# Kernel optimization log

Hardware: AMD Instinct MI355X
Metric: run time of the kernel (lower is better)

Reference implementation:

```python
import jax, jax.numpy as jnp
import numpy as np

DIM = 768
NUM_HEADS = 12
HEAD_DIM = DIM // NUM_HEADS
SCALE = HEAD_DIM ** -0.5


def setup_inputs() -> dict:
    key = jax.random.key(0)
    ks = jax.random.split(key, 9)
    B, N = 2, 4096
    s = DIM ** -0.5
    return {
        "query": jax.random.normal(ks[0], (B, N, DIM), jnp.float32),
        "key": jax.random.normal(ks[1], (B, N, DIM), jnp.float32),
        "value": jax.random.normal(ks[2], (B, N, DIM), jnp.float32),
        "Wq": jax.random.normal(ks[3], (DIM, DIM), jnp.float32) * s,
        "Wk": jax.random.normal(ks[4], (DIM, DIM), jnp.float32) * s,
        "bk": jax.random.normal(ks[5], (DIM,), jnp.float32) * 0.02,
        "Wv": jax.random.normal(ks[6], (DIM, DIM), jnp.float32) * s,
        "Wp": jax.random.normal(ks[7], (DIM, DIM), jnp.float32) * s,
        "bp": jax.random.normal(ks[8], (DIM,), jnp.float32) * 0.02,
    }


def reference(query, key, value, Wq, Wk, bk, Wv, Wp, bp):
    B, Nq, C = query.shape
    Nk = key.shape[1]
    H, D = NUM_HEADS, HEAD_DIM
    # QKV projections (qv_bias=False -> no bias on q, v; k has bias)
    q = (query @ Wq.T).reshape(B, Nq, H, D).transpose(0, 2, 1, 3)  # [B,H,Nq,D]
    k = (key @ Wk.T + bk).reshape(B, Nk, H, D).transpose(0, 2, 1, 3)
    v = (value @ Wv.T).reshape(B, Nk, H, D).transpose(0, 2, 1, 3)
    # non-standard: exact GELU applied to K before QK^T
    k = jax.nn.gelu(k, approximate=False)
    attn = jnp.einsum("bhqd,bhkd->bhqk", q, k) * SCALE
    attn = jax.nn.softmax(attn, axis=-1)
    x = jnp.einsum("bhqk,bhkd->bhqd", attn, v)
    x = x.transpose(0, 2, 1, 3).reshape(B, Nq, C)
    return x @ Wp.T + bp
```

## Files before the change

kernel.cpp:

```cpp
#include <hip/hip_runtime.h>
#include <hip/hip_bf16.h>


#define DIM 768
#define NH 12
#define HD 64
#define NTOK 4096
#define WELEM 589824u
#define TELEM 6291456u

typedef short bf16x8 __attribute__((ext_vector_type(8)));
typedef float floatx4 __attribute__((ext_vector_type(4)));
typedef unsigned short us4 __attribute__((ext_vector_type(4)));

__device__ __forceinline__ float bf2f(unsigned short u) {
    union { unsigned int i; float f; } v; v.i = ((unsigned int)u) << 16; return v.f;
}
__device__ __forceinline__ unsigned short f2bf(float f) {
    union { float f; unsigned int i; } v; v.f = f;
    unsigned int r = v.i + 0x7fffu + ((v.i >> 16) & 1u);
    return (unsigned short)(r >> 16);
}
__device__ __forceinline__ unsigned int packbf(float a, float b) {
    __hip_bfloat162 h = __float22bfloat162_rn(make_float2(a, b));
    union { __hip_bfloat162 h; unsigned int u; } cv; cv.h = h; return cv.u;
}
__device__ __forceinline__ void gl2lds16(const unsigned short* g, unsigned short* l) {
    __builtin_amdgcn_global_load_lds(
        (const __attribute__((address_space(1))) unsigned int*)g,
        (__attribute__((address_space(3))) unsigned int*)l, 16, 0, 0);
}
__device__ __forceinline__ bf16x8 ld8_f32_to_bf16(const float* p) {
    floatx4 f0 = *(const floatx4*)p;
    floatx4 f1 = *(const floatx4*)(p + 4);
    union { unsigned int u[4]; bf16x8 v; } o;
    o.u[0] = packbf(f0[0], f0[1]);
    o.u[1] = packbf(f0[2], f0[3]);
    o.u[2] = packbf(f1[0], f1[1]);
    o.u[3] = packbf(f1[2], f1[3]);
    return o.v;
}

#if __has_builtin(__builtin_amdgcn_exp2f)
#define EXPFN(x) __builtin_amdgcn_exp2f(x)
#define QSCALE 0.18033688011f
#else
#define EXPFN(x) __expf(x)
#define QSCALE 0.125f
#endif

__global__ __launch_bounds__(256) void cvt_w(
    const float* __restrict__ a, const float* __restrict__ b,
    const float* __restrict__ c, const float* __restrict__ d,
    unsigned short* __restrict__ dst)
{
    size_t i = ((size_t)blockIdx.x * 256 + threadIdx.x) * 8;
    const float* s; size_t off;
    if (i < WELEM)            { s = a; off = i; }
    else if (i < 2u * WELEM)  { s = b; off = i - WELEM; }
    else if (i < 3u * WELEM)  { s = c; off = i - 2u * WELEM; }
    else                      { s = d; off = i - 3u * WELEM; }
    *(bf16x8*)(dst + i) = ld8_f32_to_bf16(s + off);
}

__global__ __launch_bounds__(256) void cvt_in(
    const float* __restrict__ a, const float* __restrict__ b,
    const float* __restrict__ c, unsigned short* __restrict__ dst)
{
    size_t i = ((size_t)blockIdx.x * 256 + threadIdx.x) * 8;
    const float* s; size_t off;
    if (i < TELEM)            { s = a; off = i; }
    else if (i < 2u * TELEM)  { s = b; off = i - TELEM; }
    else                      { s = c; off = i - 2u * TELEM; }
    *(bf16x8*)(dst + i) = ld8_f32_to_bf16(s + off);
}

template <int A_IS_BF16>
__device__ __forceinline__ void gemm128(
    const void* __restrict__ Av, const unsigned short* __restrict__ W,
    const float* __restrict__ bias, void* __restrict__ Cv,
    int has_bias, int do_gelu, int trans, int out_f32)
{
    __shared__ unsigned short As[128 * 64];
    __shared__ unsigned short Bs[128 * 64];
    const int m0 = blockIdx.x * 128, n0 = blockIdx.y * 128;
    const int tid = threadIdx.x;
    const int w = tid >> 6, l = tid & 63;
    const int g = l >> 4, r16 = l & 15;
    const int wm = w >> 1, wn = w & 1;
    const int ro = l >> 3, c = l & 7;
    const int cswz = ((c ^ ro) & 7) * 8;

    floatx4 acc[4][4];
#pragma unroll
    for (int i = 0; i < 4; i++)
#pragma unroll
        for (int j = 0; j < 4; j++) acc[i][j] = (floatx4){0.f, 0.f, 0.f, 0.f};

    for (int k0 = 0; k0 < DIM; k0 += 64) {
#pragma unroll
        for (int q = 0; q < 4; q++) {
            int rbase = w * 32 + q * 8;
            if (A_IS_BF16) {
                gl2lds16((const unsigned short*)Av + (size_t)(m0 + rbase + ro) * DIM + k0 + cswz,
                         As + rbase * 64);
            } else {
                bf16x8 a = ld8_f32_to_bf16((const float*)Av + (size_t)(m0 + rbase + ro) * DIM + k0 + c * 8);
                *(bf16x8*)(As + (rbase + ro) * 64 + cswz) = a;
            }
            gl2lds16(W + (size_t)(n0 + rbase + ro) * DIM + k0 + cswz, Bs + rbase * 64);
        }
        __syncthreads();

#pragma unroll
        for (int kk = 0; kk < 2; kk++) {
            bf16x8 af[4], bfr[4];
            int x = r16 & 7;
#pragma unroll
            for (int i = 0; i < 4; i++)
                af[i] = *(const bf16x8*)(As + (wm * 64 + i * 16 + r16) * 64 + (((kk * 4 + g) ^ x) * 8));
#pragma unroll
            for (int j = 0; j < 4; j++)
                bfr[j] = *(const bf16x8*)(Bs + (wn * 64 + j * 16 + r16) * 64 + (((kk * 4 + g) ^ x) * 8));
#pragma unroll
            for (int i = 0; i < 4; i++)
#pragma unroll
                for (int j = 0; j < 4; j++)
                    acc[i][j] = __builtin_amdgcn_mfma_f32_16x16x32_bf16(af[i], bfr[j], acc[i][j], 0, 0, 0);
        }
        __syncthreads();
    }

    if (trans) {
        unsigned short* C = (unsigned short*)Cv;
#pragma unroll
        for (int i = 0; i < 4; i++) {
            int m = m0 + wm * 64 + i * 16 + g * 4;
            int b = m >> 12, tloc = m & 4095;
#pragma unroll
            for (int j = 0; j < 4; j++) {
                int n = n0 + wn * 64 + j * 16 + r16;
                int h = n >> 6, d = n & 63;
                union { unsigned int u[2]; us4 v; } pk;
                pk.u[0] = packbf(acc[i][j][0], acc[i][j][1]);
                pk.u[1] = packbf(acc[i][j][2], acc[i][j][3]);
                *(us4*)(C + ((size_t)(b * NH + h) * 64 + d) * NTOK + tloc) = pk.v;
            }
        }
    } else {
#pragma unroll
        for (int i = 0; i < 4; i++)
#pragma unroll
            for (int j = 0; j < 4; j++) {
                int n = n0 + wn * 64 + j * 16 + r16;
                float bv = has_bias ? bias[n] : 0.f;
#pragma unroll
                for (int r = 0; r < 4; r++) {
                    int m = m0 + wm * 64 + i * 16 + g * 4 + r;
                    float v = acc[i][j][r] + bv;
                    if (do_gelu) v = 0.5f * v * (1.f + erff(v * 0.70710678118f));
                    if (out_f32) ((float*)Cv)[(size_t)m * DIM + n] = v;
                    else ((unsigned short*)Cv)[(size_t)m * DIM + n] = f2bf(v);
                }
            }
    }
}

template <int A_IS_BF16>
__global__ __launch_bounds__(256) void qkv_gemm(
    const void* __restrict__ q_in, const void* __restrict__ k_in,
    const void* __restrict__ v_in,
    const unsigned short* __restrict__ Wq, const unsigned short* __restrict__ Wk,
    const unsigned short* __restrict__ Wv, const float* __restrict__ bk,
    unsigned short* __restrict__ Qo, unsigned short* __restrict__ Ko,
    unsigned short* __restrict__ Vto)
{
    int z = blockIdx.z;
    const void* A = (z == 0) ? q_in : (z == 1) ? k_in : v_in;
    const unsigned short* W = (z == 0) ? Wq : (z == 1) ? Wk : Wv;
    unsigned short* C = (z == 0) ? Qo : (z == 1) ? Ko : Vto;
    gemm128<A_IS_BF16>(A, W, bk, C, z == 1, z == 1, z == 2, 0);
}

__global__ __launch_bounds__(256) void out_gemm(
    const unsigned short* __restrict__ X, const unsigned short* __restrict__ Wp,
    const float* __restrict__ bp, float* __restrict__ out)
{
    gemm128<1>(X, Wp, bp, out, 1, 0, 0, 1);
}

__device__ __forceinline__ int swzf(int R) { return (R & 7) ^ ((R >> 2) & 6); }

__global__ __launch_bounds__(128, 2) void attn_kernel(
    const unsigned short* __restrict__ Q, const unsigned short* __restrict__ K,
    const unsigned short* __restrict__ Vt, unsigned short* __restrict__ X)
{
    __shared__ unsigned short Ks[2][64 * 64];
    __shared__ unsigned short Vs[2][64 * 64];
    const int qt = blockIdx.x, bh = blockIdx.y;
    const int b = bh / NH, h = bh % NH;
    const int tid = threadIdx.x;
    const int w = tid >> 6, l = tid & 63;
    const int g = l >> 4, r16 = l & 15;
    const int tokbase = b * NTOK;

    bf16x8 qfr[4][2];
#pragma unroll
    for (int qfi = 0; qfi < 4; qfi++) {
        int qrow = tokbase + qt * 128 + w * 64 + qfi * 16 + r16;
#pragma unroll
        for (int kk = 0; kk < 2; kk++) {
            bf16x8 t = *(const bf16x8*)(Q + (size_t)qrow * DIM + h * HD + kk * 32 + g * 8);
#pragma unroll
            for (int j = 0; j < 8; j++)
                t[j] = (short)f2bf(bf2f((unsigned short)t[j]) * QSCALE);
            qfr[qfi][kk] = t;
        }
    }

    int koff[4][2], voff[4][2];
#pragma unroll
    for (int ct = 0; ct < 4; ct++) {
        int krow = (ct >> 1) * 32 + (r16 >> 2) * 8 + (ct & 1) * 4 + (r16 & 3);
#pragma unroll
        for (int kk = 0; kk < 2; kk++)
            koff[ct][kk] = krow * 64 + (((kk * 4 + g) ^ swzf(krow)) * 8);
    }
#pragma unroll
    for (int dt = 0; dt < 4; dt++) {
        int vrow = dt * 16 + r16;
#pragma unroll
        for (int c = 0; c < 2; c++)
            voff[dt][c] = vrow * 64 + (((c * 4 + g) ^ swzf(vrow)) * 8);
    }

    int soff[8];
    const int srl = l >> 3, scc = l & 7;
    const int sstride = (w == 0) ? DIM : NTOK;
#pragma unroll
    for (int i = 0; i < 8; i++) {
        int row = i * 8 + srl;
        soff[i] = row * sstride + ((scc ^ swzf(row)) * 8);
    }
    const unsigned short* Kbase = K + (size_t)tokbase * DIM + h * HD;
    const unsigned short* Vbase = Vt + (size_t)bh * 64 * NTOK;

    floatx4 o[4][4];
#pragma unroll
    for (int qfi = 0; qfi < 4; qfi++)
#pragma unroll
        for (int dt = 0; dt < 4; dt++) o[qfi][dt] = (floatx4){0.f, 0.f, 0.f, 0.f};
    float lsum[4] = {0.f, 0.f, 0.f, 0.f};

    {
        const unsigned short* p = (w == 0) ? Kbase : Vbase;
        unsigned short* dst = (w == 0) ? Ks[0] : Vs[0];
#pragma unroll
        for (int i = 0; i < 8; i++) gl2lds16(p + soff[i], dst + i * 512);
    }

    for (int kt = 0; kt < NTOK / 64; kt++) {
        const int cur = kt & 1;
        __syncthreads();

        bf16x8 kr[4][2], vr[4][2];
#pragma unroll
        for (int ct = 0; ct < 4; ct++)
#pragma unroll
            for (int kk = 0; kk < 2; kk++)
                kr[ct][kk] = *(const bf16x8*)(Ks[cur] + koff[ct][kk]);
#pragma unroll
        for (int dt = 0; dt < 4; dt++)
#pragma unroll
            for (int c = 0; c < 2; c++)
                vr[dt][c] = *(const bf16x8*)(Vs[cur] + voff[dt][c]);

        if (kt + 1 < NTOK / 64) {
            int keyg = (kt + 1) * 64;
            const unsigned short* p = (w == 0) ? (Kbase + (size_t)keyg * DIM)
                                               : (Vbase + keyg);
            unsigned short* dst = (w == 0) ? Ks[cur ^ 1] : Vs[cur ^ 1];
#pragma unroll
            for (int i = 0; i < 8; i++) gl2lds16(p + soff[i], dst + i * 512);
        }

#pragma unroll
        for (int qfi = 0; qfi < 4; qfi++) {
            floatx4 s[4];
#pragma unroll
            for (int ct = 0; ct < 4; ct++) {
                floatx4 zz = (floatx4){0.f, 0.f, 0.f, 0.f};
                zz = __builtin_amdgcn_mfma_f32_16x16x32_bf16(kr[ct][0], qfr[qfi][0], zz, 0, 0, 0);
                s[ct] = __builtin_amdgcn_mfma_f32_16x16x32_bf16(kr[ct][1], qfr[qfi][1], zz, 0, 0, 0);
            }
            float ls = 0.f;
#pragma unroll
            for (int ct = 0; ct < 4; ct++)
#pragma unroll
                for (int r = 0; r < 4; r++) {
                    float p2 = EXPFN(s[ct][r]);
                    s[ct][r] = p2;
                    ls += p2;
                }
            lsum[qfi] += ls;

            unsigned int pk[4][2];
#pragma unroll
            for (int ct = 0; ct < 4; ct++) {
                pk[ct][0] = packbf(s[ct][0], s[ct][1]);
                pk[ct][1] = packbf(s[ct][2], s[ct][3]);
            }
#pragma unroll
            for (int c = 0; c < 2; c++) {
                union { unsigned int u[4]; bf16x8 v; } bf;
                bf.u[0] = pk[2 * c][0]; bf.u[1] = pk[2 * c][1];
                bf.u[2] = pk[2 * c + 1][0]; bf.u[3] = pk[2 * c + 1][1];
#pragma unroll
                for (int dt = 0; dt < 4; dt++)
                    o[qfi][dt] = __builtin_amdgcn_mfma_f32_16x16x32_bf16(vr[dt][c], bf.v, o[qfi][dt], 0, 0, 0);
            }
        }
    }

#pragma unroll
    for (int qfi = 0; qfi < 4; qfi++) {
        lsum[qfi] += __shfl_xor(lsum[qfi], 16, 64);
        lsum[qfi] += __shfl_xor(lsum[qfi], 32, 64);
    }

#pragma unroll
    for (int qfi = 0; qfi < 4; qfi++) {
        float inv = 1.f / lsum[qfi];
        int tok = tokbase + qt * 128 + w * 64 + qfi * 16 + r16;
#pragma unroll
        for (int dt = 0; dt < 4; dt++) {
            union { unsigned int u[2]; us4 v; } pkv;
            pkv.u[0] = packbf(o[qfi][dt][0] * inv, o[qfi][dt][1] * inv);
            pkv.u[1] = packbf(o[qfi][dt][2] * inv, o[qfi][dt][3] * inv);
            *(us4*)(X + (size_t)tok * DIM + h * HD + dt * 16 + g * 4) = pkv.v;
        }
    }
}

extern "C" void kernel_launch(void* const* d_in, const int* in_sizes, int n_in,
                              void* d_out, int out_size, void* d_ws, size_t ws_size,
                              hipStream_t stream) {
    const float* query = (const float*)d_in[0];
    const float* key   = (const float*)d_in[1];
    const float* value = (const float*)d_in[2];
    const float* Wq    = (const float*)d_in[3];
    const float* Wk    = (const float*)d_in[4];
    const float* bk    = (const float*)d_in[5];
    const float* Wv    = (const float*)d_in[6];
    const float* Wp    = (const float*)d_in[7];
    const float* bp    = (const float*)d_in[8];
    float* out = (float*)d_out;

    unsigned short* ws = (unsigned short*)d_ws;
    unsigned short* Wqb = ws;
    unsigned short* Wkb = Wqb + WELEM;
    unsigned short* Wvb = Wkb + WELEM;
    unsigned short* Wpb = Wvb + WELEM;
    unsigned short* Qp  = Wpb + WELEM;
    unsigned short* Kp  = Qp + TELEM;
    unsigned short* Vtp = Kp + TELEM;
    unsigned short* Xp  = Vtp + TELEM;
    unsigned short* Qbf = Xp + TELEM;
    unsigned short* Kbf = Qbf + TELEM;
    unsigned short* Vbf = Kbf + TELEM;

    const size_t base_b = ((size_t)4 * WELEM + 4 * TELEM) * 2;
    const size_t cvt_b  = (size_t)3 * TELEM * 2;
    const bool cvt_ok = ws_size >= base_b + cvt_b;

    cvt_w<<<dim3(4 * WELEM / 8 / 256), 256, 0, stream>>>(Wq, Wk, Wv, Wp, Wqb);
    if (cvt_ok) {
        cvt_in<<<dim3(3 * TELEM / 8 / 256), 256, 0, stream>>>(query, key, value, Qbf);
        qkv_gemm<1><<<dim3(64, 6, 3), 256, 0, stream>>>(Qbf, Kbf, Vbf, Wqb, Wkb, Wvb, bk, Qp, Kp, Vtp);
    } else {
        qkv_gemm<0><<<dim3(64, 6, 3), 256, 0, stream>>>(query, key, value, Wqb, Wkb, Wvb, bk, Qp, Kp, Vtp);
    }
    attn_kernel<<<dim3(32, 24), 128, 0, stream>>>(Qp, Kp, Vtp, Xp);
    out_gemm<<<dim3(64, 6), 256, 0, stream>>>(Xp, Wpb, bp, out);
}
```

Measured before the change: 331.2 us.

## Split attention block into four waves with 32 queries each

The attention kernel moves from 2 waves of 64 queries to 4 waves of 32 queries per 128-query block, with the K/V tile loads split across wave pairs. The smaller per-wave accumulators and Q fragments cut register pressure, which allows more resident waves to hide latency. The exp-sum is also split into four independent accumulators to shorten the dependency chain. In exchange, each wave now reads the full K/V tile from LDS for only half as much MFMA work, so LDS read traffic per FLOP doubles.

```diff
diff --git a/kernel.cpp b/kernel.cpp
--- a/kernel.cpp
+++ b/kernel.cpp
@@ -191,7 +191,7 @@
 
 __device__ __forceinline__ int swzf(int R) { return (R & 7) ^ ((R >> 2) & 6); }
 
-__global__ __launch_bounds__(128, 2) void attn_kernel(
+__global__ __launch_bounds__(256, 3) void attn_kernel(
     const unsigned short* __restrict__ Q, const unsigned short* __restrict__ K,
     const unsigned short* __restrict__ Vt, unsigned short* __restrict__ X)
 {
@@ -204,10 +204,10 @@
     const int g = l >> 4, r16 = l & 15;
     const int tokbase = b * NTOK;
 
-    bf16x8 qfr[4][2];
-#pragma unroll
-    for (int qfi = 0; qfi < 4; qfi++) {
-        int qrow = tokbase + qt * 128 + w * 64 + qfi * 16 + r16;
+    bf16x8 qfr[2][2];
+#pragma unroll
+    for (int qfi = 0; qfi < 2; qfi++) {
+        int qrow = tokbase + qt * 128 + w * 32 + qfi * 16 + r16;
 #pragma unroll
         for (int kk = 0; kk < 2; kk++) {
             bf16x8 t = *(const bf16x8*)(Q + (size_t)qrow * DIM + h * HD + kk * 32 + g * 8);
@@ -234,29 +234,30 @@
             voff[dt][c] = vrow * 64 + (((c * 4 + g) ^ swzf(vrow)) * 8);
     }
 
-    int soff[8];
+    const int kv = w >> 1, half = w & 1;
+    int soff[4];
     const int srl = l >> 3, scc = l & 7;
-    const int sstride = (w == 0) ? DIM : NTOK;
-#pragma unroll
-    for (int i = 0; i < 8; i++) {
-        int row = i * 8 + srl;
+    const int sstride = (kv == 0) ? DIM : NTOK;
+#pragma unroll
+    for (int i = 0; i < 4; i++) {
+        int row = half * 32 + i * 8 + srl;
         soff[i] = row * sstride + ((scc ^ swzf(row)) * 8);
     }
     const unsigned short* Kbase = K + (size_t)tokbase * DIM + h * HD;
     const unsigned short* Vbase = Vt + (size_t)bh * 64 * NTOK;
 
-    floatx4 o[4][4];
-#pragma unroll
-    for (int qfi = 0; qfi < 4; qfi++)
+    floatx4 o[2][4];
+#pragma unroll
+    for (int qfi = 0; qfi < 2; qfi++)
 #pragma unroll
         for (int dt = 0; dt < 4; dt++) o[qfi][dt] = (floatx4){0.f, 0.f, 0.f, 0.f};
-    float lsum[4] = {0.f, 0.f, 0.f, 0.f};
+    float lsum[2] = {0.f, 0.f};
 
     {
-        const unsigned short* p = (w == 0) ? Kbase : Vbase;
-        unsigned short* dst = (w == 0) ? Ks[0] : Vs[0];
-#pragma unroll
-        for (int i = 0; i < 8; i++) gl2lds16(p + soff[i], dst + i * 512);
+        const unsigned short* p = (kv == 0) ? Kbase : Vbase;
+        unsigned short* dst = ((kv == 0) ? Ks[0] : Vs[0]) + half * 2048;
+#pragma unroll
+        for (int i = 0; i < 4; i++) gl2lds16(p + soff[i], dst + i * 512);
     }
 
     for (int kt = 0; kt < NTOK / 64; kt++) {
@@ -277,15 +278,15 @@
 
         if (kt + 1 < NTOK / 64) {
             int keyg = (kt + 1) * 64;
-            const unsigned short* p = (w == 0) ? (Kbase + (size_t)keyg * DIM)
-                                               : (Vbase + keyg);
-            unsigned short* dst = (w == 0) ? Ks[cur ^ 1] : Vs[cur ^ 1];
-#pragma unroll
-            for (int i = 0; i < 8; i++) gl2lds16(p + soff[i], dst + i * 512);
-        }
-
-#pragma unroll
-        for (int qfi = 0; qfi < 4; qfi++) {
+            const unsigned short* p = (kv == 0) ? (Kbase + (size_t)keyg * DIM)
+                                                : (Vbase + keyg);
+            unsigned short* dst = ((kv == 0) ? Ks[cur ^ 1] : Vs[cur ^ 1]) + half * 2048;
+#pragma unroll
+            for (int i = 0; i < 4; i++) gl2lds16(p + soff[i], dst + i * 512);
+        }
+
+#pragma unroll
+        for (int qfi = 0; qfi < 2; qfi++) {
             floatx4 s[4];
 #pragma unroll
             for (int ct = 0; ct < 4; ct++) {
@@ -293,16 +294,17 @@
                 zz = __builtin_amdgcn_mfma_f32_16x16x32_bf16(kr[ct][0], qfr[qfi][0], zz, 0, 0, 0);
                 s[ct] = __builtin_amdgcn_mfma_f32_16x16x32_bf16(kr[ct][1], qfr[qfi][1], zz, 0, 0, 0);
             }
-            float ls = 0.f;
-#pragma unroll
-            for (int ct = 0; ct < 4; ct++)
-#pragma unroll
-                for (int r = 0; r < 4; r++) {
-                    float p2 = EXPFN(s[ct][r]);
-                    s[ct][r] = p2;
-                    ls += p2;
-                }
-            lsum[qfi] += ls;
+            float ls0 = 0.f, ls1 = 0.f, ls2 = 0.f, ls3 = 0.f;
+#pragma unroll
+            for (int ct = 0; ct < 4; ct++) {
+                float p0 = EXPFN(s[ct][0]);
+                float p1 = EXPFN(s[ct][1]);
+                float p2 = EXPFN(s[ct][2]);
+                float p3 = EXPFN(s[ct][3]);
+                s[ct][0] = p0; s[ct][1] = p1; s[ct][2] = p2; s[ct][3] = p3;
+                ls0 += p0; ls1 += p1; ls2 += p2; ls3 += p3;
+            }
+            lsum[qfi] += (ls0 + ls1) + (ls2 + ls3);
 
             unsigned int pk[4][2];
 #pragma unroll
@@ -323,15 +325,15 @@
     }
 
 #pragma unroll
-    for (int qfi = 0; qfi < 4; qfi++) {
+    for (int qfi = 0; qfi < 2; qfi++) {
         lsum[qfi] += __shfl_xor(lsum[qfi], 16, 64);
         lsum[qfi] += __shfl_xor(lsum[qfi], 32, 64);
     }
 
 #pragma unroll
-    for (int qfi = 0; qfi < 4; qfi++) {
+    for (int qfi = 0; qfi < 2; qfi++) {
         float inv = 1.f / lsum[qfi];
-        int tok = tokbase + qt * 128 + w * 64 + qfi * 16 + r16;
+        int tok = tokbase + qt * 128 + w * 32 + qfi * 16 + r16;
 #pragma unroll
         for (int dt = 0; dt < 4; dt++) {
             union { unsigned int u[2]; us4 v; } pkv;
@@ -380,6 +382,6 @@
     } else {
         qkv_gemm<0><<<dim3(64, 6, 3), 256, 0, stream>>>(query, key, value, Wqb, Wkb, Wvb, bk, Qp, Kp, Vtp);
     }
-    attn_kernel<<<dim3(32, 24), 128, 0, stream>>>(Qp, Kp, Vtp, Xp);
+    attn_kernel<<<dim3(32, 24), 256, 0, stream>>>(Qp, Kp, Vtp, Xp);
     out_gemm<<<dim3(64, 6), 256, 0, stream>>>(Xp, Wpb, bp, out);
 }
```

Result: faster. 311.2 us (-6.0%).
